# Kernel optimization log

Hardware: AMD Instinct MI355X
Metric: run time of the kernel (lower is better)

The kernel has to match this reference:

```python
import jax, jax.numpy as jnp
import numpy as np

TAU = 2.0      # spikingjelly LIFNode default tau
V_TH = 1.0     # default v_threshold
ALPHA = 4.0    # default surrogate.Sigmoid alpha
H, HL = 8, 2   # num_heads, local_heads

@jax.custom_vjp
def spike(u):
    # Heaviside: fire when membrane potential >= threshold (u = v - v_th)
    return (u >= 0.0).astype(u.dtype)

def _spike_fwd(u):
    return spike(u), u

def _spike_bwd(u, g):
    s = jax.nn.sigmoid(ALPHA * u)
    return (g * ALPHA * s * (1.0 - s),)

spike.defvjp(_spike_fwd, _spike_bwd)

def lif(x):
    # Multi-step LIF, decay_input=False, v_reset=0.0 (hard reset), detach_reset=True.
    # Charge: v = v - (v - 0)/tau + x ; spike when v >= v_th ; reset v -> 0 where spiked.
    decay = 1.0 - 1.0 / TAU
    def step(v, xt):
        v = v * decay + xt
        s = spike(v - V_TH)
        v = v * (1.0 - jax.lax.stop_gradient(s))  # detach_reset
        return v, s
    _, spikes = jax.lax.scan(step, jnp.zeros_like(x[0]), x)
    return spikes

def setup_inputs() -> dict:
    key = jax.random.key(0)
    ks = jax.random.split(key, 5)
    T, B, C, D = 4, 8, 512, 768
    hd = D // H            # 96
    mkv = hd * HL          # 192 (GQA kv projection width)
    scale = 0.1            # keeps LIF membrane potentials near threshold
    return {
        "x": jax.random.normal(ks[0], (T, B, C, D), jnp.float32),
        "q_w": jax.random.normal(ks[1], (D, D), jnp.float32) * scale,
        "k_w": jax.random.normal(ks[2], (mkv, D), jnp.float32) * scale,
        "v_w": jax.random.normal(ks[3], (mkv, D), jnp.float32) * scale,
        "wo_w": jax.random.normal(ks[4], (D, D), jnp.float32) * scale,
    }

def reference(x, q_w, k_w, v_w, wo_w):
    T, B, C, D = x.shape
    hd = D // H
    n_rep = H // HL
    xs = lif(x)  # proj_lif
    # q: (T,B,C,D) -> (T,B,H,C,hd)
    q = lif(xs @ q_w.T).reshape(T, B, C, H, hd).transpose(0, 1, 3, 2, 4)
    # k,v: (T,B,C,mkv) -> repeat_interleave over kv heads -> (T,B,H,C,hd)
    k = lif(xs @ k_w.T).reshape(T, B, C, HL, hd)
    k = jnp.repeat(k, n_rep, axis=3).transpose(0, 1, 3, 2, 4)
    v = lif(xs @ v_w.T).reshape(T, B, C, HL, hd)
    v = jnp.repeat(v, n_rep, axis=3).transpose(0, 1, 3, 2, 4)
    # softmax-free attention: (q k^T) * 0.1 @ v
    scores = jnp.einsum('tbhqd,tbhkd->tbhqk', q, k) * 0.1
    out = jnp.einsum('tbhqk,tbhkd->tbhqd', scores, v)
    # (T,B,H,C,hd) -> (T,B,C,D)
    out = out.transpose(0, 1, 3, 2, 4).reshape(T, B, C, D)
    return out @ wo_w.T
```

## Files before the change

kernel.cpp:

```cpp
#include <hip/hip_runtime.h>

typedef __bf16 bf16;
typedef __bf16 bf16x8 __attribute__((ext_vector_type(8)));
typedef float f32x4 __attribute__((ext_vector_type(4)));

#define T_ 4
#define B_ 8
#define C_ 512
#define D_ 768
#define H_ 8
#define HL_ 2
#define HD_ 96
#define MKV_ 192
#define M2_ 4096
#define BCD_ 3145728
#define M3_ 16384
#define NCOMB 1152
#define SUSP_CAP 65536
#define SUSP_WIN 2e-4f

__device__ __forceinline__ void gld16(const bf16* g, bf16* l) {
    __builtin_amdgcn_global_load_lds(
        (const __attribute__((address_space(1))) unsigned int*)g,
        (__attribute__((address_space(3))) unsigned int*)l, 16, 0, 0);
}

__global__ __launch_bounds__(256) void prep_kernel(
    const float* __restrict__ x, const float* __restrict__ q_w,
    const float* __restrict__ k_w, const float* __restrict__ v_w,
    const float* __restrict__ wo_w, bf16* __restrict__ xs,
    bf16* __restrict__ whi, bf16* __restrict__ wlo, bf16* __restrict__ wo_bf,
    unsigned* __restrict__ susp)
{
    const int t0 = blockIdx.x * 256 + threadIdx.x;
    const int stride = gridDim.x * 256;
    if (t0 == 0) susp[0] = 0;
    for (int i = t0; i < BCD_; i += stride) {
        double v = 0.0;
        #pragma unroll
        for (int t = 0; t < T_; ++t) {
            v = v * 0.5 + (double)x[(size_t)t * BCD_ + i];
            float s = (v >= 1.0) ? 1.0f : 0.0f;
            xs[(size_t)t * BCD_ + i] = (bf16)s;
            if (s != 0.0f) v = 0.0;
        }
    }
    for (int i = t0; i < NCOMB * D_; i += stride) {
        int row = i / D_, col = i - row * D_;
        float v;
        if (row < 768)      v = q_w[(size_t)row * D_ + col];
        else if (row < 960) v = k_w[(size_t)(row - 768) * D_ + col];
        else                v = v_w[(size_t)(row - 960) * D_ + col];
        bf16 h = (bf16)v;
        whi[i] = h;
        wlo[i] = (bf16)(v - (float)h);
    }
    for (int i = t0; i < D_ * D_; i += stride)
        wo_bf[i] = (bf16)wo_w[i];
}

__global__ __launch_bounds__(256, 3) void proj_lif_kernel(
    const bf16* __restrict__ xs, const bf16* __restrict__ Whi,
    const bf16* __restrict__ Wlo,
    bf16* __restrict__ q_sp, bf16* __restrict__ k_sp, bf16* __restrict__ v_sp,
    unsigned* __restrict__ susp)
{
    __shared__ __align__(16) bf16 Alds[2][T_][64 * 32];
    __shared__ __align__(16) bf16 Hlds[2][64 * 32];
    __shared__ __align__(16) bf16 Llds[2][64 * 32];

    const int tid  = threadIdx.x;
    const int wave = tid >> 6, lane = tid & 63;
    const int m16  = lane & 15, quad = lane >> 4;
    const int wm   = wave >> 1, wn = wave & 1;

    const int bid   = blockIdx.y * 64 + blockIdx.x;
    const int xcd   = bid & 7;
    const int local = bid >> 3;
    const int m0    = ((xcd << 3) | (local & 7)) * 64;
    const int n0    = (local >> 3) * 64;

    const int colb = n0 + wn * 32;
    bf16* outp; int Nloc, cb;
    if (colb < 768)      { outp = q_sp; Nloc = 768; cb = colb; }
    else if (colb < 960) { outp = k_sp; Nloc = 192; cb = colb - 768; }
    else                 { outp = v_sp; Nloc = 192; cb = colb - 960; }

    f32x4 acc[T_][2][2];
    #pragma unroll
    for (int t = 0; t < T_; t++)
        #pragma unroll
        for (int a = 0; a < 2; a++)
            #pragma unroll
            for (int b = 0; b < 2; b++) { f32x4 z = {0.f,0.f,0.f,0.f}; acc[t][a][b] = z; }

    auto stage = [&](int buf, int k0) {
        const int row = tid >> 2;
        const int seg = (tid & 3) ^ ((tid >> 3) & 3);
        #pragma unroll
        for (int j = 0; j < T_; j++)
            gld16(xs + (size_t)(j * M2_ + m0 + row) * D_ + k0 + seg * 8,
                  &Alds[buf][j][tid * 8]);
        gld16(Whi + (size_t)(n0 + row) * D_ + k0 + seg * 8, &Hlds[buf][tid * 8]);
        gld16(Wlo + (size_t)(n0 + row) * D_ + k0 + seg * 8, &Llds[buf][tid * 8]);
    };

    stage(0, 0);
    asm volatile("s_waitcnt vmcnt(0)" ::: "memory");
    __builtin_amdgcn_s_barrier();

    int cur = 0;
    for (int s = 0; s < 24; ++s) {
        if (s + 1 < 24) stage(cur ^ 1, (s + 1) * 32);

        bf16x8 a[T_][2], bh[2], bl[2];
        #pragma unroll
        for (int mi = 0; mi < 2; mi++) {
            int row = wm * 32 + mi * 16 + m16;
            int off = row * 32 + (((quad) ^ ((row >> 1) & 3)) * 8);
            #pragma unroll
            for (int t = 0; t < T_; t++)
                a[t][mi] = *(const bf16x8*)&Alds[cur][t][off];
        }
        #pragma unroll
        for (int ni = 0; ni < 2; ni++) {
            int row = wn * 32 + ni * 16 + m16;
            int off = row * 32 + (((quad) ^ ((row >> 1) & 3)) * 8);
            bh[ni] = *(const bf16x8*)&Hlds[cur][off];
            bl[ni] = *(const bf16x8*)&Llds[cur][off];
        }
        __builtin_amdgcn_s_setprio(1);
        #pragma unroll
        for (int ni = 0; ni < 2; ni++)
            #pragma unroll
            for (int t = 0; t < T_; t++)
                #pragma unroll
                for (int mi = 0; mi < 2; mi++) {
                    acc[t][mi][ni] = __builtin_amdgcn_mfma_f32_16x16x32_bf16(a[t][mi], bh[ni], acc[t][mi][ni], 0, 0, 0);
                    acc[t][mi][ni] = __builtin_amdgcn_mfma_f32_16x16x32_bf16(a[t][mi], bl[ni], acc[t][mi][ni], 0, 0, 0);
                }
        __builtin_amdgcn_s_setprio(0);

        asm volatile("s_waitcnt vmcnt(0)" ::: "memory");
        __builtin_amdgcn_s_barrier();
        cur ^= 1;
    }

    #pragma unroll
    for (int mi = 0; mi < 2; mi++)
        #pragma unroll
        for (int ni = 0; ni < 2; ni++)
            #pragma unroll
            for (int rr = 0; rr < 4; rr++) {
                int row = m0 + wm * 32 + mi * 16 + quad * 4 + rr;
                int lc  = cb + ni * 16 + m16;
                float v = 0.f;
                bool suspect = false;
                #pragma unroll
                for (int t = 0; t < T_; t++) {
                    v = v * 0.5f + acc[t][mi][ni][rr];
                    float d = v - 1.0f;
                    if (fabsf(d) < SUSP_WIN) suspect = true;
                    float sp = (d >= 0.f) ? 1.f : 0.f;
                    v *= (1.f - sp);
                    outp[(size_t)(t * M2_ + row) * Nloc + lc] = (bf16)sp;
                }
                if (suspect) {
                    int ccol = n0 + wn * 32 + ni * 16 + m16;
                    unsigned idx = atomicAdd(susp, 1u);
                    if (idx < SUSP_CAP) susp[1 + idx] = (unsigned)(row * 2048 + ccol);
                }
            }
}

__global__ __launch_bounds__(256) void fixup_kernel(
    const bf16* __restrict__ xs, const float* __restrict__ q_w,
    const float* __restrict__ k_w, const float* __restrict__ v_w,
    bf16* __restrict__ q_sp, bf16* __restrict__ k_sp, bf16* __restrict__ v_sp,
    const unsigned* __restrict__ susp)
{
    unsigned count = susp[0];
    if (count > SUSP_CAP) count = SUSP_CAP;
    const int lane = threadIdx.x & 63;
    const int wid  = (blockIdx.x * blockDim.x + threadIdx.x) >> 6;
    const int nw   = (gridDim.x * blockDim.x) >> 6;
    for (unsigned i = wid; i < count; i += nw) {
        unsigned e = susp[1 + i];
        int row = e >> 11, col = e & 2047;
        const float* W; bf16* outp; int Nloc, lc;
        if (col < 768)      { W = q_w + (size_t)col * D_;         outp = q_sp; Nloc = 768; lc = col; }
        else if (col < 960) { W = k_w + (size_t)(col - 768) * D_; outp = k_sp; Nloc = 192; lc = col - 768; }
        else                { W = v_w + (size_t)(col - 960) * D_; outp = v_sp; Nloc = 192; lc = col - 960; }
        double v = 0.0;
        for (int t = 0; t < T_; ++t) {
            const bf16* ar = xs + (size_t)(t * M2_ + row) * D_;
            double y = 0.0;
            for (int k = lane; k < D_; k += 64)
                y += (double)(float)ar[k] * (double)W[k];
            #pragma unroll
            for (int off = 1; off < 64; off <<= 1)
                y += __shfl_xor(y, off);
            v = v * 0.5 + y;
            unsigned sp = (v >= 1.0) ? 1u : 0u;
            if (lane == 0) outp[(size_t)(t * M2_ + row) * Nloc + lc] = (bf16)(float)sp;
            if (sp) v = 0.0;
        }
    }
}

__global__ __launch_bounds__(256) void ktv_kernel(
    const bf16* __restrict__ k_sp, const bf16* __restrict__ v_sp,
    float* __restrict__ M_part)
{
    const int g    = blockIdx.x;
    const int cc   = blockIdx.y;
    const int kvh  = g % HL_;
    const int tb   = g / HL_;
    const int wave = threadIdx.x >> 6;
    const int lane = threadIdx.x & 63;
    const int m16  = lane & 15, quad = lane >> 4;

    __shared__ __align__(16) bf16 klds[96 * 40];
    __shared__ __align__(16) bf16 vlds[96 * 40];

    f32x4 acc[9];
    #pragma unroll
    for (int i = 0; i < 9; i++) { f32x4 z = {0.f,0.f,0.f,0.f}; acc[i] = z; }

    const bf16* kbase = k_sp + ((size_t)tb * C_ + cc * 64) * MKV_ + kvh * HD_;
    const bf16* vbase = v_sp + ((size_t)tb * C_ + cc * 64) * MKV_ + kvh * HD_;

    for (int c0 = 0; c0 < 64; c0 += 32) {
        __syncthreads();
        for (int ci = threadIdx.x; ci < 768; ci += 256) {
            int arr = ci & 1;
            int pos = ci >> 1;
            int c = pos / 12, seg = pos - c * 12;
            const bf16* src = (arr ? vbase : kbase) + (size_t)(c0 + c) * MKV_ + seg * 8;
            bf16x8 val = *(const bf16x8*)src;
            bf16* dst = arr ? vlds : klds;
            #pragma unroll
            for (int e = 0; e < 8; e++)
                dst[(seg * 8 + e) * 40 + c] = val[e];
        }
        __syncthreads();
        #pragma unroll
        for (int i = 0; i < 9; i++) {
            int tile = wave + i * 4;
            int mt = tile / 6, nt = tile % 6;
            bf16x8 a = *(const bf16x8*)(&klds[(mt * 16 + m16) * 40 + quad * 8]);
            bf16x8 b = *(const bf16x8*)(&vlds[(nt * 16 + m16) * 40 + quad * 8]);
            acc[i] = __builtin_amdgcn_mfma_f32_16x16x32_bf16(a, b, acc[i], 0, 0, 0);
        }
    }
    float* op = M_part + ((size_t)cc * 64 + g) * HD_ * HD_;
    #pragma unroll
    for (int i = 0; i < 9; i++) {
        int tile = wave + i * 4;
        int mt = tile / 6, nt = tile % 6;
        #pragma unroll
        for (int r = 0; r < 4; r++) {
            int d = mt * 16 + quad * 4 + r;
            int j = nt * 16 + m16;
            op[(size_t)j * HD_ + d] = acc[i][r];
        }
    }
}

__global__ __launch_bounds__(256) void cvtM_kernel(
    const float* __restrict__ M_part, bf16* __restrict__ M_hi,
    bf16* __restrict__ M_lo)
{
    int i = blockIdx.x * 256 + threadIdx.x;
    if (i >= 64 * HD_ * HD_) return;
    float m = 0.f;
    #pragma unroll
    for (int j = 0; j < 8; j++)
        m += M_part[i + (size_t)j * 589824];
    bf16 h = (bf16)m;
    M_hi[i] = h;
    M_lo[i] = (bf16)(m - (float)h);
}

__global__ __launch_bounds__(256) void qm_kernel(
    const bf16* __restrict__ q_sp, const bf16* __restrict__ M_hi,
    const bf16* __restrict__ M_lo, bf16* __restrict__ out_attn)
{
    const int tbh  = blockIdx.x;
    const int h    = tbh % H_;
    const int tb   = tbh / H_;
    const int g    = tb * HL_ + (h >> 2);
    const int wave = threadIdx.x >> 6;
    const int lane = threadIdx.x & 63;
    const int m16  = lane & 15, quad = lane >> 4;
    const int cw   = blockIdx.y * 128 + wave * 32;

    __shared__ __align__(16) bf16 Mh[96 * 104];
    __shared__ __align__(16) bf16 Ml[96 * 104];
    {
        const bf16* gh = M_hi + (size_t)g * HD_ * HD_;
        const bf16* gl = M_lo + (size_t)g * HD_ * HD_;
        #pragma unroll
        for (int j = 0; j < 5; j++) {
            int ci = j * 256 + threadIdx.x;
            if (ci < 1152) {
                int row = ci / 12, seg = ci % 12;
                *(bf16x8*)&Mh[row * 104 + seg * 8] = *(const bf16x8*)(gh + row * HD_ + seg * 8);
                *(bf16x8*)&Ml[row * 104 + seg * 8] = *(const bf16x8*)(gl + row * HD_ + seg * 8);
            }
        }
    }
    __syncthreads();

    f32x4 acc[2][6];
    #pragma unroll
    for (int mi = 0; mi < 2; mi++)
        #pragma unroll
        for (int nt = 0; nt < 6; nt++) { f32x4 z = {0.f,0.f,0.f,0.f}; acc[mi][nt] = z; }

    #pragma unroll
    for (int ks = 0; ks < 3; ++ks) {
        bf16x8 a[2];
        #pragma unroll
        for (int mi = 0; mi < 2; mi++)
            a[mi] = *(const bf16x8*)(q_sp + ((size_t)(tb * C_ + cw + mi * 16 + m16)) * D_
                                     + h * HD_ + ks * 32 + quad * 8);
        #pragma unroll
        for (int nt = 0; nt < 6; ++nt) {
            bf16x8 bh = *(const bf16x8*)&Mh[(nt * 16 + m16) * 104 + ks * 32 + quad * 8];
            bf16x8 bl = *(const bf16x8*)&Ml[(nt * 16 + m16) * 104 + ks * 32 + quad * 8];
            #pragma unroll
            for (int mi = 0; mi < 2; mi++) {
                acc[mi][nt] = __builtin_amdgcn_mfma_f32_16x16x32_bf16(a[mi], bh, acc[mi][nt], 0, 0, 0);
                acc[mi][nt] = __builtin_amdgcn_mfma_f32_16x16x32_bf16(a[mi], bl, acc[mi][nt], 0, 0, 0);
            }
        }
    }
    #pragma unroll
    for (int mi = 0; mi < 2; mi++)
        #pragma unroll
        for (int nt = 0; nt < 6; nt++)
            #pragma unroll
            for (int r = 0; r < 4; r++) {
                int c = cw + mi * 16 + quad * 4 + r;
                int j = nt * 16 + m16;
                out_attn[((size_t)(tb * C_ + c)) * D_ + h * HD_ + j] = (bf16)(0.1f * acc[mi][nt][r]);
            }
}

__global__ __launch_bounds__(256) void final_gemm_kernel(
    const bf16* __restrict__ A, const bf16* __restrict__ W, float* __restrict__ out)
{
    __shared__ __align__(16) bf16 Alds[128 * 64];
    __shared__ __align__(16) bf16 Blds[128 * 64];
    const int tid  = threadIdx.x;
    const int wave = tid >> 6, lane = tid & 63;
    const int m16  = lane & 15, quad = lane >> 4;
    const int wm   = wave >> 1, wn = wave & 1;
    const int m0   = blockIdx.x * 128, n0 = blockIdx.y * 128;

    f32x4 acc[4][4];
    #pragma unroll
    for (int a = 0; a < 4; a++)
        #pragma unroll
        for (int b = 0; b < 4; b++) { f32x4 z = {0.f,0.f,0.f,0.f}; acc[a][b] = z; }

    for (int k0 = 0; k0 < D_; k0 += 64) {
        __syncthreads();
        #pragma unroll
        for (int j = 0; j < 4; j++) {
            int ci = j * 256 + tid;
            int row = ci >> 3, slot = ci & 7;
            int seg = slot ^ ((row >> 1) & 7);
            gld16(A + (size_t)(m0 + row) * D_ + k0 + seg * 8, Alds + ci * 8);
            gld16(W + (size_t)(n0 + row) * D_ + k0 + seg * 8, Blds + ci * 8);
        }
        __syncthreads();
        #pragma unroll
        for (int kc = 0; kc < 2; kc++) {
            bf16x8 a[4], b[4];
            #pragma unroll
            for (int mi = 0; mi < 4; mi++) {
                int row = wm * 64 + mi * 16 + m16;
                a[mi] = *(const bf16x8*)&Alds[row * 64 + (((kc * 4 + quad) ^ ((row >> 1) & 7)) * 8)];
            }
            #pragma unroll
            for (int ni = 0; ni < 4; ni++) {
                int row = wn * 64 + ni * 16 + m16;
                b[ni] = *(const bf16x8*)&Blds[row * 64 + (((kc * 4 + quad) ^ ((row >> 1) & 7)) * 8)];
            }
            #pragma unroll
            for (int mi = 0; mi < 4; mi++)
                #pragma unroll
                for (int ni = 0; ni < 4; ni++)
                    acc[mi][ni] = __builtin_amdgcn_mfma_f32_16x16x32_bf16(a[mi], b[ni], acc[mi][ni], 0, 0, 0);
        }
    }
    #pragma unroll
    for (int mi = 0; mi < 4; mi++)
        #pragma unroll
        for (int ni = 0; ni < 4; ni++)
            #pragma unroll
            for (int r = 0; r < 4; r++) {
                int row = m0 + wm * 64 + mi * 16 + quad * 4 + r;
                int col = n0 + wn * 64 + ni * 16 + m16;
                out[(size_t)row * D_ + col] = acc[mi][ni][r];
            }
}

extern "C" void kernel_launch(void* const* d_in, const int* in_sizes, int n_in,
                              void* d_out, int out_size, void* d_ws, size_t ws_size,
                              hipStream_t stream) {
    const float* x    = (const float*)d_in[0];
    const float* q_w  = (const float*)d_in[1];
    const float* k_w  = (const float*)d_in[2];
    const float* v_w  = (const float*)d_in[3];
    const float* wo_w = (const float*)d_in[4];
    float* out = (float*)d_out;

    char* ws = (char*)d_ws;
    bf16* xs    = (bf16*)(ws);
    bf16* q_sp  = (bf16*)(ws + 25165824);
    bf16* k_sp  = (bf16*)(ws + 50331648);
    bf16* v_sp  = (bf16*)(ws + 56623104);
    bf16* whi   = (bf16*)(ws + 62914560);
    bf16* wlo   = (bf16*)(ws + 64684032);
    bf16* wo_bf = (bf16*)(ws + 66453504);
    bf16* M_hi  = (bf16*)(ws + 67633152);
    bf16* M_lo  = (bf16*)(ws + 68812800);
    unsigned* susp = (unsigned*)(ws + 69992448);
    bf16* out_attn = xs;
    float* M_part  = out;

    hipLaunchKernelGGL(prep_kernel, dim3(2048), dim3(256), 0, stream,
                       x, q_w, k_w, v_w, wo_w, xs, whi, wlo, wo_bf, susp);
    hipLaunchKernelGGL(proj_lif_kernel, dim3(M2_ / 64, NCOMB / 64), dim3(256), 0, stream,
                       xs, whi, wlo, q_sp, k_sp, v_sp, susp);
    hipLaunchKernelGGL(fixup_kernel, dim3(256), dim3(256), 0, stream,
                       xs, q_w, k_w, v_w, q_sp, k_sp, v_sp, susp);
    hipLaunchKernelGGL(ktv_kernel, dim3(T_ * B_ * HL_, 8), dim3(256), 0, stream,
                       k_sp, v_sp, M_part);
    hipLaunchKernelGGL(cvtM_kernel, dim3((64 * HD_ * HD_ + 255) / 256), dim3(256), 0, stream,
                       M_part, M_hi, M_lo);
    hipLaunchKernelGGL(qm_kernel, dim3(T_ * B_ * H_, C_ / 128), dim3(256), 0, stream,
                       q_sp, M_hi, M_lo, out_attn);
    hipLaunchKernelGGL(final_gemm_kernel, dim3(M3_ / 128, D_ / 128), dim3(256), 0, stream,
                       out_attn, wo_bf, out);
}
```

Before: 276.9 us.

## Restructure projection GEMM main loop into two-stage prefetch with partial vmcnt waits

Rewrites the projection GEMM K-loop so that two LDS stages stay in flight. Each step copies its fragments into registers, waits on LDS reads and a barrier, then issues the global-to-LDS prefetch for K-step s+2 into the freed buffer before running the MFMAs. The end-of-step wait becomes a partial vmcnt(6) instead of vmcnt(0), so the next tile's loads stay outstanding during compute. This adds a barrier per step and makes correctness depend on the exact load count per stage (six).

After: 266.0 us. -4.0%, faster.

```diff
diff --git a/kernel.cpp b/kernel.cpp
--- a/kernel.cpp
+++ b/kernel.cpp
@@ -65,9 +65,12 @@
     bf16* __restrict__ q_sp, bf16* __restrict__ k_sp, bf16* __restrict__ v_sp,
     unsigned* __restrict__ susp)
 {
-    __shared__ __align__(16) bf16 Alds[2][T_][64 * 32];
-    __shared__ __align__(16) bf16 Hlds[2][64 * 32];
-    __shared__ __align__(16) bf16 Llds[2][64 * 32];
+    __shared__ __align__(16) bf16 A0[T_][64 * 32];
+    __shared__ __align__(16) bf16 A1[T_][64 * 32];
+    __shared__ __align__(16) bf16 H0[64 * 32];
+    __shared__ __align__(16) bf16 H1[64 * 32];
+    __shared__ __align__(16) bf16 L0[64 * 32];
+    __shared__ __align__(16) bf16 L1[64 * 32];
 
     const int tid  = threadIdx.x;
     const int wave = tid >> 6, lane = tid & 63;
@@ -94,57 +97,93 @@
             #pragma unroll
             for (int b = 0; b < 2; b++) { f32x4 z = {0.f,0.f,0.f,0.f}; acc[t][a][b] = z; }
 
-    auto stage = [&](int buf, int k0) {
-        const int row = tid >> 2;
-        const int seg = (tid & 3) ^ ((tid >> 3) & 3);
-        #pragma unroll
-        for (int j = 0; j < T_; j++)
-            gld16(xs + (size_t)(j * M2_ + m0 + row) * D_ + k0 + seg * 8,
-                  &Alds[buf][j][tid * 8]);
-        gld16(Whi + (size_t)(n0 + row) * D_ + k0 + seg * 8, &Hlds[buf][tid * 8]);
-        gld16(Wlo + (size_t)(n0 + row) * D_ + k0 + seg * 8, &Llds[buf][tid * 8]);
-    };
-
-    stage(0, 0);
-    asm volatile("s_waitcnt vmcnt(0)" ::: "memory");
-    __builtin_amdgcn_s_barrier();
-
-    int cur = 0;
-    for (int s = 0; s < 24; ++s) {
-        if (s + 1 < 24) stage(cur ^ 1, (s + 1) * 32);
-
-        bf16x8 a[T_][2], bh[2], bl[2];
-        #pragma unroll
-        for (int mi = 0; mi < 2; mi++) {
-            int row = wm * 32 + mi * 16 + m16;
-            int off = row * 32 + (((quad) ^ ((row >> 1) & 3)) * 8);
-            #pragma unroll
-            for (int t = 0; t < T_; t++)
-                a[t][mi] = *(const bf16x8*)&Alds[cur][t][off];
-        }
-        #pragma unroll
-        for (int ni = 0; ni < 2; ni++) {
-            int row = wn * 32 + ni * 16 + m16;
-            int off = row * 32 + (((quad) ^ ((row >> 1) & 3)) * 8);
-            bh[ni] = *(const bf16x8*)&Hlds[cur][off];
-            bl[ni] = *(const bf16x8*)&Llds[cur][off];
-        }
-        __builtin_amdgcn_s_setprio(1);
-        #pragma unroll
-        for (int ni = 0; ni < 2; ni++)
-            #pragma unroll
-            for (int t = 0; t < T_; t++)
-                #pragma unroll
-                for (int mi = 0; mi < 2; mi++) {
-                    acc[t][mi][ni] = __builtin_amdgcn_mfma_f32_16x16x32_bf16(a[t][mi], bh[ni], acc[t][mi][ni], 0, 0, 0);
-                    acc[t][mi][ni] = __builtin_amdgcn_mfma_f32_16x16x32_bf16(a[t][mi], bl[ni], acc[t][mi][ni], 0, 0, 0);
-                }
-        __builtin_amdgcn_s_setprio(0);
-
-        asm volatile("s_waitcnt vmcnt(0)" ::: "memory");
-        __builtin_amdgcn_s_barrier();
-        cur ^= 1;
-    }
+    const int srow = tid >> 2;
+    const int sseg = (tid & 3) ^ ((tid >> 3) & 3);
+
+#define STAGE(Ab, Hb, Lb, k0) do {                                            \
+    _Pragma("unroll")                                                         \
+    for (int t = 0; t < T_; t++)                                              \
+        gld16(xs + (size_t)(t * M2_ + m0 + srow) * D_ + (k0) + sseg * 8,      \
+              &Ab[t][tid * 8]);                                               \
+    gld16(Whi + (size_t)(n0 + srow) * D_ + (k0) + sseg * 8, &Hb[tid * 8]);    \
+    gld16(Wlo + (size_t)(n0 + srow) * D_ + (k0) + sseg * 8, &Lb[tid * 8]);    \
+} while (0)
+
+    bf16x8 a[T_][2], bh[2], bl[2];
+
+#define LOADREGS(Ab, Hb, Lb) do {                                             \
+    _Pragma("unroll")                                                         \
+    for (int mi = 0; mi < 2; mi++) {                                          \
+        int row = wm * 32 + mi * 16 + m16;                                    \
+        int off = row * 32 + ((quad ^ ((row >> 1) & 3)) * 8);                 \
+        _Pragma("unroll")                                                     \
+        for (int t = 0; t < T_; t++) a[t][mi] = *(const bf16x8*)&Ab[t][off];  \
+    }                                                                         \
+    _Pragma("unroll")                                                         \
+    for (int ni = 0; ni < 2; ni++) {                                          \
+        int row = wn * 32 + ni * 16 + m16;                                    \
+        int off = row * 32 + ((quad ^ ((row >> 1) & 3)) * 8);                 \
+        bh[ni] = *(const bf16x8*)&Hb[off];                                    \
+        bl[ni] = *(const bf16x8*)&Lb[off];                                    \
+    }                                                                         \
+} while (0)
+
+#define DOMFMA() do {                                                         \
+    __builtin_amdgcn_s_setprio(1);                                            \
+    _Pragma("unroll")                                                         \
+    for (int ni = 0; ni < 2; ni++)                                            \
+        _Pragma("unroll")                                                     \
+        for (int t = 0; t < T_; t++)                                          \
+            _Pragma("unroll")                                                 \
+            for (int mi = 0; mi < 2; mi++) {                                  \
+                acc[t][mi][ni] = __builtin_amdgcn_mfma_f32_16x16x32_bf16(     \
+                    a[t][mi], bh[ni], acc[t][mi][ni], 0, 0, 0);               \
+                acc[t][mi][ni] = __builtin_amdgcn_mfma_f32_16x16x32_bf16(     \
+                    a[t][mi], bl[ni], acc[t][mi][ni], 0, 0, 0);               \
+            }                                                                 \
+    __builtin_amdgcn_s_setprio(0);                                            \
+} while (0)
+
+#define READS_DONE() do {                                                     \
+    asm volatile("s_waitcnt lgkmcnt(0)" ::: "memory");                        \
+    __builtin_amdgcn_s_barrier();                                             \
+    __builtin_amdgcn_sched_barrier(0);                                        \
+} while (0)
+
+#define NEXT_READY(N) do {                                                    \
+    asm volatile("s_waitcnt vmcnt(" #N ")" ::: "memory");                     \
+    __builtin_amdgcn_s_barrier();                                             \
+} while (0)
+
+    STAGE(A0, H0, L0, 0);
+    STAGE(A1, H1, L1, 32);
+    NEXT_READY(6);
+
+    for (int s = 0; s < 22; s += 2) {
+        LOADREGS(A0, H0, L0);
+        READS_DONE();
+        STAGE(A0, H0, L0, (s + 2) * 32);
+        DOMFMA();
+        NEXT_READY(6);
+
+        LOADREGS(A1, H1, L1);
+        READS_DONE();
+        STAGE(A1, H1, L1, (s + 3) * 32);
+        DOMFMA();
+        NEXT_READY(6);
+    }
+    LOADREGS(A0, H0, L0);
+    READS_DONE();
+    DOMFMA();
+    NEXT_READY(0);
+    LOADREGS(A1, H1, L1);
+    DOMFMA();
+
+#undef STAGE
+#undef LOADREGS
+#undef DOMFMA
+#undef READS_DONE
+#undef NEXT_READY
 
     #pragma unroll
     for (int mi = 0; mi < 2; mi++)
```
